# Optimization experiments

Measured on AMD Instinct MI355X. Metric: run time of the kernel, lower is better.

The kernel has to match this reference:

```python
import jax, jax.numpy as jnp
import numpy as np

K = 3
PAD = 1


def bilinear_gather(xr, py, px):
    # xr: [B, G, H, W, C] channels-last per offset group; py/px: [B, G, H, W] sample coords
    B, G, H, W, C = xr.shape
    y0 = jnp.floor(py)
    x0 = jnp.floor(px)
    wy = py - y0
    wx = px - x0
    y0i = y0.astype(jnp.int32)
    x0i = x0.astype(jnp.int32)
    bi = jnp.arange(B)[:, None, None, None]
    gi = jnp.arange(G)[None, :, None, None]
    out = jnp.zeros(py.shape + (C,), xr.dtype)
    corners = (
        (0, 0, (1 - wy) * (1 - wx)),
        (0, 1, (1 - wy) * wx),
        (1, 0, wy * (1 - wx)),
        (1, 1, wy * wx),
    )
    for dy_, dx_, w in corners:
        yy = y0i + dy_
        xx = x0i + dx_
        valid = ((yy >= 0) & (yy < H) & (xx >= 0) & (xx < W)).astype(xr.dtype)
        yc = jnp.clip(yy, 0, H - 1)
        xc = jnp.clip(xx, 0, W - 1)
        v = xr[bi, gi, yc, xc]  # [B,G,H,W,C]
        out = out + (w * valid)[..., None] * v
    return out


def setup_inputs() -> dict:
    key = jax.random.key(0)
    k1, k2, k3, k4, k5 = jax.random.split(key, 5)
    B, Cin, H, W = 4, 64, 256, 256
    G, OC = 8, 64
    KK = K * K
    x = jax.random.normal(k1, (B, Cin, H, W), jnp.float32)
    offset = jax.random.normal(k2, (B, 2, G * KK, H, W), jnp.float32)
    mask = jax.random.normal(k3, (B, G * KK, H, W), jnp.float32)
    weight = jax.random.normal(k4, (OC, Cin // G, K, K), jnp.float32) * 0.05
    bias = jax.random.normal(k5, (OC,), jnp.float32) * 0.01
    return {"x": x, "offset": offset, "mask": mask, "weight": weight, "bias": bias}


def reference(x, offset, mask, weight, bias):
    B, Cin, H, W = x.shape
    OC, Cpg, _, _ = weight.shape
    G = Cin // Cpg          # conv groups == offset groups here
    OPG = OC // G
    KK = K * K
    # replicate module's permute(0,2,1,3,4).flip(1).view(b,-1,fh,fw):
    # pair axis (dy,dx) is input dim 1; combined (group,tap) axis is reversed
    off = jnp.flip(offset, axis=2)                      # [B,2,G*KK,H,W]
    dy = off[:, 0].reshape(B, G, KK, H, W)
    dx = off[:, 1].reshape(B, G, KK, H, W)
    m = jax.nn.sigmoid(mask).reshape(B, G, KK, H, W)
    xr = x.reshape(B, G, Cpg, H, W).transpose(0, 1, 3, 4, 2)  # [B,G,H,W,Cpg]
    wg = weight.reshape(G, OPG, Cpg, K, K)
    iy = jnp.arange(H, dtype=x.dtype)[None, None, :, None]
    ix = jnp.arange(W, dtype=x.dtype)[None, None, None, :]
    out = jnp.zeros((B, G, OPG, H, W), x.dtype)
    for t in range(KK):  # fixed small loop over kernel taps
        ki, kj = t // K, t % K
        py = iy - PAD + ki + dy[:, :, t]
        px = ix - PAD + kj + dx[:, :, t]
        s = bilinear_gather(xr, py, px) * m[:, :, t][..., None]  # [B,G,H,W,Cpg]
        out = out + jnp.einsum('bghwc,gdc->bgdhw', s, wg[:, :, :, ki, kj])
    return out.reshape(B, OC, H, W) + bias[None, :, None, None]
```

## Files before the change

### kernel.cpp

```cpp
#include <hip/hip_runtime.h>
#include <hip/hip_fp16.h>


#define KSZ 3
#define PAD 1

static constexpr int B   = 4;
static constexpr int Cin = 64;
static constexpr int H   = 256;
static constexpr int W   = 256;
static constexpr int G   = 8;
static constexpr int OC  = 64;
static constexpr int KK  = KSZ * KSZ;
static constexpr int Cpg = Cin / G;
static constexpr int OPG = OC / G;
static constexpr int HW  = H * W;
static constexpr int NXCD = 8;

static constexpr int WROWS  = 13;
static constexpr int WUP    = 5;
static constexpr int WPITCH = 257;

typedef _Float16 f16x8  __attribute__((ext_vector_type(8)));
typedef float    f32x16 __attribute__((ext_vector_type(16)));

union U4H {
    uint4 u;
    __half2 h2[4];
    _Float16 h[8];
    f16x8 v;
};

__global__ __launch_bounds__(256) void transpose_kernel(
    const float* __restrict__ x, uint4* __restrict__ xt)
{
    const int h = blockIdx.x, g = blockIdx.y, b = blockIdx.z;
    const int w = threadIdx.x;
    const int pix = h * W + w;
    const float* src = x + (size_t)(b * Cin + g * Cpg) * HW + pix;
    U4H v;
#pragma unroll
    for (int c = 0; c < 8; ++c) v.h[c] = (_Float16)src[(size_t)c * HW];
    xt[(size_t)(b * G + g) * HW + pix] = v.u;
}

__global__ __launch_bounds__(512) void dcn_kernel(
    const uint4* __restrict__ xt,
    const float* __restrict__ offset,
    const float* __restrict__ mask,
    const float* __restrict__ weight,
    const float* __restrict__ bias,
    float* __restrict__ out)
{
    __shared__ uint4 win[WROWS * WPITCH];

    const unsigned id = blockIdx.x;
    const unsigned wl = (id & (NXCD - 1)) * (gridDim.x / NXCD) + (id >> 3);
    const int p  = wl & (H / 2 - 1);
    const int bg = wl >> 7;
    const int g  = bg & (G - 1);
    const int b  = bg >> 3;
    const int h_base = 2 * p;

    const int tid  = threadIdx.x;
    const int lane = tid & 63;
    const int wave = tid >> 6;
    const int row_sel = wave >> 2;
    const int wv   = wave & 3;
    const int hi   = lane >> 5;
    const int lp   = lane & 31;

    const int h  = h_base + row_sel;
    const int h0 = h_base - WUP;

    const uint4* xb = xt + (size_t)(b * G + g) * HW;

#pragma unroll
    for (int it = 0; it < 7; ++it) {
        const int k = it * 512 + tid;
        if (k < WROWS * 256) {
            const int i   = k >> 8;
            const int col = k & 255;
            const int wr  = min(max(h0 + i, 0), H - 1);
            win[i * WPITCH + col] = xb[wr * W + col];
        }
    }

    f16x8 afrag[5];
#pragma unroll
    for (int m = 0; m < 5; ++m) {
        f16x8 a = {};
        const int t = 2 * m + hi;
        if (lp < OPG && t < KK) {
            const float* wp = weight + (size_t)(g * OPG + lp) * Cpg * KK + t;
#pragma unroll
            for (int c = 0; c < 8; ++c) a[c] = (_Float16)wp[c * KK];
        }
        afrag[m] = a;
    }

    const float* offy = offset + (size_t)(b * 2 + 0) * (G * KK) * HW;
    const float* offx = offset + (size_t)(b * 2 + 1) * (G * KK) * HW;
    const float* mk   = mask + (size_t)b * (G * KK) * HW;

    float dyv[2][5], dxv[2][5], msv[2][5];
#pragma unroll
    for (int tile = 0; tile < 2; ++tile) {
        const int wq  = wv * 64 + tile * 32 + lp;
        const int pix = h * W + wq;
#pragma unroll
        for (int m = 0; m < 5; ++m) {
            const int t  = 2 * m + hi;
            const int tt = (t > 8) ? 8 : t;
            const int idx0 = G * KK - 1 - (g * KK + tt);
            dyv[tile][m] = offy[(size_t)idx0 * HW + pix];
            dxv[tile][m] = offx[(size_t)idx0 * HW + pix];
            const float mv = mk[(size_t)(g * KK + tt) * HW + pix];
            float s = 1.0f / (1.0f + __expf(-mv));
            msv[tile][m] = (t <= 8) ? s : 0.0f;
        }
    }

    __syncthreads();

    auto sample = [&](int t, int wq, float dy, float dx, float msig) -> f16x8 {
        const int tt = (t > 8) ? 8 : t;
        const int ki = (tt >= 3) + (tt >= 6);
        const int kj = tt - 3 * ki;

        const float py = (float)(h - PAD + ki) + dy;
        const float px = (float)(wq - PAD + kj) + dx;
        const float y0f = floorf(py), x0f = floorf(px);
        const float wy = py - y0f, wx = px - x0f;
        const int y0 = (int)y0f, x0 = (int)x0f;
        const bool vy0 = (y0 >= 0) & (y0 < H), vy1 = (y0 + 1 >= 0) & (y0 + 1 < H);
        const bool vx0 = (x0 >= 0) & (x0 < W), vx1 = (x0 + 1 >= 0) & (x0 + 1 < W);

        const float u   = vy0 ? (1.f - wy) * msig : 0.f;
        const float v   = vy1 ? wy * msig : 0.f;
        const float cx0 = vx0 ? (1.f - wx) : 0.f;
        const float cx1 = vx1 ? wx : 0.f;

        const int iy0 = y0 - h0;
        const int iy1 = iy0 + 1;
        const int i0 = min(max(iy0, 0), WROWS - 1);
        const int i1 = min(max(iy1, 0), WROWS - 1);
        const int xc0 = min(max(x0, 0), W - 1);
        const int xc1 = min(max(x0 + 1, 0), W - 1);

        uint4 v00 = win[i0 * WPITCH + xc0];
        uint4 v01 = win[i0 * WPITCH + xc1];
        uint4 v10 = win[i1 * WPITCH + xc0];
        uint4 v11 = win[i1 * WPITCH + xc1];

        const bool bad = (vy0 & ((unsigned)iy0 > (unsigned)(WROWS - 1))) |
                         (vy1 & ((unsigned)iy1 > (unsigned)(WROWS - 1)));
        if (__builtin_expect(__any((int)bad), 0)) {
            if (bad) {
                const int yc0 = min(max(y0, 0), H - 1);
                const int yc1 = min(max(y0 + 1, 0), H - 1);
                v00 = xb[yc0 * W + xc0];
                v01 = xb[yc0 * W + xc1];
                v10 = xb[yc1 * W + xc0];
                v11 = xb[yc1 * W + xc1];
            }
        }

        const float w00 = u * cx0, w01 = u * cx1, w10 = v * cx0, w11 = v * cx1;
        U4H a, bq, c, d; a.u = v00; bq.u = v01; c.u = v10; d.u = v11;
        const __half2 hw00 = __float2half2_rn(w00);
        const __half2 hw01 = __float2half2_rn(w01);
        const __half2 hw10 = __float2half2_rn(w10);
        const __half2 hw11 = __float2half2_rn(w11);
        U4H s;
#pragma unroll
        for (int i = 0; i < 4; ++i)
            s.h2[i] = __hfma2(hw00, a.h2[i],
                      __hfma2(hw01, bq.h2[i],
                      __hfma2(hw10, c.h2[i],
                      __hmul2(hw11, d.h2[i]))));
        return s.v;
    };

    f32x16 acc0 = {};
    f32x16 acc1 = {};
    {
        const int wq = wv * 64 + lp;
#pragma unroll
        for (int m = 0; m < 5; ++m)
            acc0 = __builtin_amdgcn_mfma_f32_32x32x16_f16(
                afrag[m], sample(2 * m + hi, wq, dyv[0][m], dxv[0][m], msv[0][m]), acc0, 0, 0, 0);
    }
    {
        const int wq = wv * 64 + 32 + lp;
#pragma unroll
        for (int m = 0; m < 5; ++m)
            acc1 = __builtin_amdgcn_mfma_f32_32x32x16_f16(
                afrag[m], sample(2 * m + hi, wq, dyv[1][m], dxv[1][m], msv[1][m]), acc1, 0, 0, 0);
    }

#pragma unroll
    for (int tile = 0; tile < 2; ++tile) {
        const int wq = wv * 64 + tile * 32 + lp;
#pragma unroll
        for (int r = 0; r < 4; ++r) {
            const int dd = r + 4 * hi;
            const float v = (tile == 0 ? acc0[r] : acc1[r]) + bias[g * OPG + dd];
            out[((size_t)b * OC + g * OPG + dd) * HW + h * W + wq] = v;
        }
    }
}

extern "C" void kernel_launch(void* const* d_in, const int* in_sizes, int n_in,
                              void* d_out, int out_size, void* d_ws, size_t ws_size,
                              hipStream_t stream) {
    const float* x      = (const float*)d_in[0];
    const float* offset = (const float*)d_in[1];
    const float* mask   = (const float*)d_in[2];
    const float* weight = (const float*)d_in[3];
    const float* bias   = (const float*)d_in[4];
    float* out = (float*)d_out;
    uint4* xt  = (uint4*)d_ws;

    dim3 tgrid(H, G, B);
    transpose_kernel<<<tgrid, dim3(256), 0, stream>>>(x, xt);
    dcn_kernel<<<dim3(B * G * H / 2), dim3(512), 0, stream>>>(xt, offset, mask, weight, bias, out);
}
```

Measured before the change: 115.7 us.

## Use one output row per block, prepack weight fragments, add fast in-window sampling path

The DCN kernel now runs 256-thread blocks that each handle a single output row, instead of 512-thread blocks covering two rows. The shared window shrinks to 12 rows and launch bounds request 3 blocks per CU, aiming for higher occupancy. Weight MFMA fragments are packed once into f16 by a new small kernel, so each block loads them directly rather than doing strided fp32 loads and conversions. The sampler adds a wave-uniform fast path that skips per-corner clamping and masking when all lanes fall inside the image and window. The trade-off is that the row halo is loaded twice as often, which adds global traffic and an extra kernel launch.

```diff
diff --git a/kernel.cpp b/kernel.cpp
--- a/kernel.cpp
+++ b/kernel.cpp
@@ -17,7 +17,7 @@
 static constexpr int HW  = H * W;
 static constexpr int NXCD = 8;
 
-static constexpr int WROWS  = 13;
+static constexpr int WROWS  = 12;
 static constexpr int WUP    = 5;
 static constexpr int WPITCH = 257;
 
@@ -44,11 +44,32 @@
     xt[(size_t)(b * G + g) * HW + pix] = v.u;
 }
 
-__global__ __launch_bounds__(512) void dcn_kernel(
+__global__ __launch_bounds__(320) void prep_weights(
+    const float* __restrict__ weight, uint4* __restrict__ wfrag)
+{
+    const int g    = blockIdx.x;
+    const int tid  = threadIdx.x;
+    const int m    = tid >> 6;
+    const int lane = tid & 63;
+    const int hi   = lane >> 5;
+    const int lp   = lane & 31;
+    const int t    = 2 * m + hi;
+    U4H a;
+#pragma unroll
+    for (int c = 0; c < 8; ++c) {
+        float v = 0.0f;
+        if (lp < OPG && t < KK)
+            v = weight[((size_t)(g * OPG + lp) * Cpg + c) * KK + t];
+        a.h[c] = (_Float16)v;
+    }
+    wfrag[((size_t)g * 5 + m) * 64 + lane] = a.u;
+}
+
+__global__ __launch_bounds__(256, 3) void dcn_kernel(
     const uint4* __restrict__ xt,
+    const uint4* __restrict__ wfrag,
     const float* __restrict__ offset,
     const float* __restrict__ mask,
-    const float* __restrict__ weight,
     const float* __restrict__ bias,
     float* __restrict__ out)
 {
@@ -56,47 +77,34 @@
 
     const unsigned id = blockIdx.x;
     const unsigned wl = (id & (NXCD - 1)) * (gridDim.x / NXCD) + (id >> 3);
-    const int p  = wl & (H / 2 - 1);
-    const int bg = wl >> 7;
+    const int h  = wl & (H - 1);
+    const int bg = wl >> 8;
     const int g  = bg & (G - 1);
     const int b  = bg >> 3;
-    const int h_base = 2 * p;
 
     const int tid  = threadIdx.x;
     const int lane = tid & 63;
     const int wave = tid >> 6;
-    const int row_sel = wave >> 2;
-    const int wv   = wave & 3;
     const int hi   = lane >> 5;
     const int lp   = lane & 31;
 
-    const int h  = h_base + row_sel;
-    const int h0 = h_base - WUP;
-
     const uint4* xb = xt + (size_t)(b * G + g) * HW;
-
-#pragma unroll
-    for (int it = 0; it < 7; ++it) {
-        const int k = it * 512 + tid;
-        if (k < WROWS * 256) {
-            const int i   = k >> 8;
-            const int col = k & 255;
-            const int wr  = min(max(h0 + i, 0), H - 1);
-            win[i * WPITCH + col] = xb[wr * W + col];
-        }
+    const int h0 = h - WUP;
+
+#pragma unroll
+    for (int i = 0; i < WROWS; ++i) {
+        const int wr = min(max(h0 + i, 0), H - 1);
+        win[i * WPITCH + tid] = xb[wr * W + tid];
     }
 
     f16x8 afrag[5];
-#pragma unroll
-    for (int m = 0; m < 5; ++m) {
-        f16x8 a = {};
-        const int t = 2 * m + hi;
-        if (lp < OPG && t < KK) {
-            const float* wp = weight + (size_t)(g * OPG + lp) * Cpg * KK + t;
-#pragma unroll
-            for (int c = 0; c < 8; ++c) a[c] = (_Float16)wp[c * KK];
-        }
-        afrag[m] = a;
+    {
+        const uint4* wf = wfrag + (size_t)g * 5 * 64 + lane;
+#pragma unroll
+        for (int m = 0; m < 5; ++m) {
+            U4H tmp; tmp.u = wf[m * 64];
+            afrag[m] = tmp.v;
+        }
     }
 
     const float* offy = offset + (size_t)(b * 2 + 0) * (G * KK) * HW;
@@ -106,7 +114,7 @@
     float dyv[2][5], dxv[2][5], msv[2][5];
 #pragma unroll
     for (int tile = 0; tile < 2; ++tile) {
-        const int wq  = wv * 64 + tile * 32 + lp;
+        const int wq  = wave * 64 + tile * 32 + lp;
         const int pix = h * W + wq;
 #pragma unroll
         for (int m = 0; m < 5; ++m) {
@@ -133,40 +141,52 @@
         const float y0f = floorf(py), x0f = floorf(px);
         const float wy = py - y0f, wx = px - x0f;
         const int y0 = (int)y0f, x0 = (int)x0f;
-        const bool vy0 = (y0 >= 0) & (y0 < H), vy1 = (y0 + 1 >= 0) & (y0 + 1 < H);
-        const bool vx0 = (x0 >= 0) & (x0 < W), vx1 = (x0 + 1 >= 0) & (x0 + 1 < W);
-
-        const float u   = vy0 ? (1.f - wy) * msig : 0.f;
-        const float v   = vy1 ? wy * msig : 0.f;
-        const float cx0 = vx0 ? (1.f - wx) : 0.f;
-        const float cx1 = vx1 ? wx : 0.f;
-
-        const int iy0 = y0 - h0;
-        const int iy1 = iy0 + 1;
-        const int i0 = min(max(iy0, 0), WROWS - 1);
-        const int i1 = min(max(iy1, 0), WROWS - 1);
-        const int xc0 = min(max(x0, 0), W - 1);
-        const int xc1 = min(max(x0 + 1, 0), W - 1);
-
-        uint4 v00 = win[i0 * WPITCH + xc0];
-        uint4 v01 = win[i0 * WPITCH + xc1];
-        uint4 v10 = win[i1 * WPITCH + xc0];
-        uint4 v11 = win[i1 * WPITCH + xc1];
-
-        const bool bad = (vy0 & ((unsigned)iy0 > (unsigned)(WROWS - 1))) |
-                         (vy1 & ((unsigned)iy1 > (unsigned)(WROWS - 1)));
-        if (__builtin_expect(__any((int)bad), 0)) {
-            if (bad) {
-                const int yc0 = min(max(y0, 0), H - 1);
-                const int yc1 = min(max(y0 + 1, 0), H - 1);
-                v00 = xb[yc0 * W + xc0];
-                v01 = xb[yc0 * W + xc1];
-                v10 = xb[yc1 * W + xc0];
-                v11 = xb[yc1 * W + xc1];
+        const int iy0 = y0 - h0, iy1 = iy0 + 1;
+
+        float w00, w01, w10, w11;
+        uint4 v00, v01, v10, v11;
+
+        const bool ok = (y0 >= 0) & (y0 + 1 < H) & (x0 >= 0) & (x0 + 1 < W) &
+                        ((unsigned)iy0 <= (unsigned)(WROWS - 2));
+        if (__all((int)ok)) {
+            const float u = (1.f - wy) * msig, v = wy * msig;
+            w00 = u * (1.f - wx); w01 = u * wx;
+            w10 = v * (1.f - wx); w11 = v * wx;
+            const int a0 = iy0 * WPITCH + x0;
+            v00 = win[a0];          v01 = win[a0 + 1];
+            v10 = win[a0 + WPITCH]; v11 = win[a0 + WPITCH + 1];
+        } else {
+            const bool vy0 = (y0 >= 0) & (y0 < H), vy1 = (y0 + 1 >= 0) & (y0 + 1 < H);
+            const bool vx0 = (x0 >= 0) & (x0 < W), vx1 = (x0 + 1 >= 0) & (x0 + 1 < W);
+            const float u   = vy0 ? (1.f - wy) * msig : 0.f;
+            const float v   = vy1 ? wy * msig : 0.f;
+            const float cx0 = vx0 ? (1.f - wx) : 0.f;
+            const float cx1 = vx1 ? wx : 0.f;
+            w00 = u * cx0; w01 = u * cx1; w10 = v * cx0; w11 = v * cx1;
+
+            const int i0 = min(max(iy0, 0), WROWS - 1);
+            const int i1 = min(max(iy1, 0), WROWS - 1);
+            const int xc0 = min(max(x0, 0), W - 1);
+            const int xc1 = min(max(x0 + 1, 0), W - 1);
+            v00 = win[i0 * WPITCH + xc0];
+            v01 = win[i0 * WPITCH + xc1];
+            v10 = win[i1 * WPITCH + xc0];
+            v11 = win[i1 * WPITCH + xc1];
+
+            const bool bad = (vy0 & ((unsigned)iy0 > (unsigned)(WROWS - 1))) |
+                             (vy1 & ((unsigned)iy1 > (unsigned)(WROWS - 1)));
+            if (__builtin_expect(__any((int)bad), 0)) {
+                if (bad) {
+                    const int yc0 = min(max(y0, 0), H - 1);
+                    const int yc1 = min(max(y0 + 1, 0), H - 1);
+                    v00 = xb[yc0 * W + xc0];
+                    v01 = xb[yc0 * W + xc1];
+                    v10 = xb[yc1 * W + xc0];
+                    v11 = xb[yc1 * W + xc1];
+                }
             }
         }
 
-        const float w00 = u * cx0, w01 = u * cx1, w10 = v * cx0, w11 = v * cx1;
         U4H a, bq, c, d; a.u = v00; bq.u = v01; c.u = v10; d.u = v11;
         const __half2 hw00 = __float2half2_rn(w00);
         const __half2 hw01 = __float2half2_rn(w01);
@@ -185,14 +205,14 @@
     f32x16 acc0 = {};
     f32x16 acc1 = {};
     {
-        const int wq = wv * 64 + lp;
+        const int wq = wave * 64 + lp;
 #pragma unroll
         for (int m = 0; m < 5; ++m)
             acc0 = __builtin_amdgcn_mfma_f32_32x32x16_f16(
                 afrag[m], sample(2 * m + hi, wq, dyv[0][m], dxv[0][m], msv[0][m]), acc0, 0, 0, 0);
     }
     {
-        const int wq = wv * 64 + 32 + lp;
+        const int wq = wave * 64 + 32 + lp;
 #pragma unroll
         for (int m = 0; m < 5; ++m)
             acc1 = __builtin_amdgcn_mfma_f32_32x32x16_f16(
@@ -201,7 +221,7 @@
 
 #pragma unroll
     for (int tile = 0; tile < 2; ++tile) {
-        const int wq = wv * 64 + tile * 32 + lp;
+        const int wq = wave * 64 + tile * 32 + lp;
 #pragma unroll
         for (int r = 0; r < 4; ++r) {
             const int dd = r + 4 * hi;
@@ -220,9 +240,12 @@
     const float* weight = (const float*)d_in[3];
     const float* bias   = (const float*)d_in[4];
     float* out = (float*)d_out;
-    uint4* xt  = (uint4*)d_ws;
+
+    uint4* xt    = (uint4*)d_ws;
+    uint4* wfrag = (uint4*)((char*)d_ws + (size_t)B * G * HW * 16);
 
     dim3 tgrid(H, G, B);
     transpose_kernel<<<tgrid, dim3(256), 0, stream>>>(x, xt);
-    dcn_kernel<<<dim3(B * G * H / 2), dim3(512), 0, stream>>>(xt, offset, mask, weight, bias, out);
-}
+    prep_weights<<<dim3(G), dim3(320), 0, stream>>>(weight, wfrag);
+    dcn_kernel<<<dim3(B * G * H), dim3(256), 0, stream>>>(xt, wfrag, offset, mask, bias, out);
+}
```

Measured after the change: 96.08 us. 16.9% less time.
